# Performance work log

Measured on AMD Instinct MI355X. Metric: run time of the kernel, lower is better.

The kernel has to match this reference:

```python
import jax, jax.numpy as jnp
import numpy as np

H = 12          # num_heads
LENS_T = 64     # template tokens
LENS_S = 256    # search tokens
KEEP = int(0.7 * LENS_S)  # 179 kept search tokens


def _ln(x, s, b):
    mu = jnp.mean(x, axis=-1, keepdims=True)
    var = jnp.mean(jnp.square(x - mu), axis=-1, keepdims=True)
    return (x - mu) / jnp.sqrt(var + 1e-5) * s + b


def setup_inputs() -> dict:
    key = jax.random.key(0)
    ks = jax.random.split(key, 8)
    B, C, Hh = 32, 768, 3072
    N = LENS_T + LENS_S
    w = lambda k, shape: jax.random.normal(k, shape, jnp.float32) * 0.02
    return {
        "x": jax.random.normal(ks[0], (B, N, C), jnp.float32),
        "global_index_t": jnp.tile(jnp.arange(LENS_T, dtype=jnp.int32), (B, 1)),
        "global_index_s": jnp.tile(jnp.arange(LENS_S, dtype=jnp.int32), (B, 1)),
        "norm1_s": jnp.ones((C,), jnp.float32), "norm1_b": jnp.zeros((C,), jnp.float32),
        "qkv_w": w(ks[1], (C, 3 * C)), "qkv_b": jnp.zeros((3 * C,), jnp.float32),
        "proj_w": w(ks[2], (C, C)), "proj_b": jnp.zeros((C,), jnp.float32),
        "norm2_s": jnp.ones((C,), jnp.float32), "norm2_b": jnp.zeros((C,), jnp.float32),
        "fc1_w": w(ks[3], (C, Hh)), "fc1_b": jnp.zeros((Hh,), jnp.float32),
        "fc2_w": w(ks[4], (Hh, C)), "fc2_b": jnp.zeros((C,), jnp.float32),
        "gcn_w": w(ks[5], (C, C)), "gcn_b": jnp.zeros((C,), jnp.float32),
        "norm3_s": jnp.ones((C,), jnp.float32), "norm3_b": jnp.zeros((C,), jnp.float32),
    }


def reference(x, global_index_t, global_index_s,
              norm1_s, norm1_b, qkv_w, qkv_b, proj_w, proj_b,
              norm2_s, norm2_b, fc1_w, fc1_b, fc2_w, fc2_b,
              gcn_w, gcn_b, norm3_s, norm3_b):
    B, N, C = x.shape
    hd = C // H
    scale = hd ** -0.5

    # --- attention (attn weights explicitly materialized) ---
    h = _ln(x, norm1_s, norm1_b)
    qkv = (h @ qkv_w + qkv_b).reshape(B, N, 3, H, hd).transpose(2, 0, 3, 1, 4)
    q, k, v = qkv[0], qkv[1], qkv[2]                      # [B,H,N,hd]
    attn = jax.nn.softmax(jnp.einsum('bhqd,bhkd->bhqk', q, k) * scale, axis=-1)
    xa = jnp.einsum('bhqk,bhkd->bhqd', attn, v).transpose(0, 2, 1, 3).reshape(B, N, C)
    xa = xa @ proj_w + proj_b
    x = x + xa

    # --- MLP ---
    x_res = x
    h2 = _ln(x, norm2_s, norm2_b)
    h2 = jax.nn.gelu(h2 @ fc1_w + fc1_b, approximate=False) @ fc2_w + fc2_b
    x = x_res + h2

    # --- GCN using template<->search attention as adjacency ---
    # adjacency = [[0, w_ts], [w_ts^T, 0]]; exploit block sparsity instead of
    # materializing the dense [B,N,N] matrix.
    w_ts = jnp.sum(attn[:, :, :LENS_T, LENS_T:], axis=1) / H   # [B,T,S]
    w_ts = jax.nn.softmax(w_ts, axis=2)
    support = x @ gcn_w + gcn_b
    out_t = jnp.einsum('bts,bsd->btd', w_ts, support[:, LENS_T:])   # top block
    out_s = jnp.einsum('bts,btd->bsd', w_ts, support[:, :LENS_T])   # bottom block
    x = jnp.concatenate([out_t, out_s], axis=1)
    x = x + _ln(x, norm3_s, norm3_b)

    # --- top-k token pruning on search tokens ---
    score_s = jnp.mean(attn[:, :, :LENS_T, LENS_T:], axis=(1, 2))   # [B,S]
    order = jnp.argsort(-score_s, axis=1)
    keep_indices = order[:, :KEEP]
    removed_index_s = order[:, KEEP:]
    gs_new = jnp.take_along_axis(global_index_s, keep_indices, axis=1)
    idx = jnp.concatenate([global_index_t.astype(jnp.int32), keep_indices + LENS_T], axis=1)
    x = jnp.take_along_axis(x, jnp.broadcast_to(idx[..., None], (B, idx.shape[1], C)), axis=1)
    return (x, global_index_t, gs_new, removed_index_s, attn)
```

## Files before the change

kernel.cpp:

```cpp
#include <hip/hip_runtime.h>
#include <math.h>

#define NKEEP 179
#define NREM  77
#define NOUT_ROWS 243

typedef __bf16 bf16x8 __attribute__((ext_vector_type(8)));
typedef float f32x4 __attribute__((ext_vector_type(4)));

__device__ __forceinline__ unsigned short f2bf(float f) {
  unsigned u = __builtin_bit_cast(unsigned, f);
  u = (u + 0x7FFFu + ((u >> 16) & 1u)) >> 16;
  return (unsigned short)u;
}

__device__ __forceinline__ void gload_lds16(const void* g, void* l) {
  __builtin_amdgcn_global_load_lds((const __attribute__((address_space(1))) void*)g,
                                   (__attribute__((address_space(3))) void*)l,
                                   16, 0, 0);
}

template<int RESID, int OUTMODE>
__global__ __launch_bounds__(256)
void ln_kernel(const float* __restrict__ in, const float* __restrict__ gs,
               const float* __restrict__ gb, void* __restrict__ outp,
               void* __restrict__ outp2) {
  int row = blockIdx.x;
  const float* p = in + (size_t)row * 768;
  int tid = threadIdx.x;
  float v0 = p[tid], v1 = p[tid + 256], v2 = p[tid + 512];
  __shared__ double rs[256], rq[256];
  double d0 = v0, d1 = v1, d2 = v2;
  rs[tid] = d0 + d1 + d2;
  rq[tid] = d0 * d0 + d1 * d1 + d2 * d2;
  __syncthreads();
  for (int st = 128; st > 0; st >>= 1) {
    if (tid < st) { rs[tid] += rs[tid + st]; rq[tid] += rq[tid + st]; }
    __syncthreads();
  }
  double mu  = rs[0] * (1.0 / 768.0);
  double var = rq[0] * (1.0 / 768.0) - mu * mu;
  float rstd = (float)rsqrt(var + 1e-5);
  float muf = (float)mu;
  float y0 = (v0 - muf) * rstd * gs[tid]       + gb[tid];
  float y1 = (v1 - muf) * rstd * gs[tid + 256] + gb[tid + 256];
  float y2 = (v2 - muf) * rstd * gs[tid + 512] + gb[tid + 512];
  if (RESID) { y0 += v0; y1 += v1; y2 += v2; }
  if (OUTMODE == 0 || OUTMODE == 2) {
    float* o = (float*)outp + (size_t)row * 768;
    o[tid] = y0; o[tid + 256] = y1; o[tid + 512] = y2;
  }
  if (OUTMODE == 1) {
    unsigned short* o = (unsigned short*)outp + (size_t)row * 768;
    o[tid] = f2bf(y0); o[tid + 256] = f2bf(y1); o[tid + 512] = f2bf(y2);
  }
  if (OUTMODE == 2) {
    unsigned short* o = (unsigned short*)outp2 + (size_t)row * 768;
    o[tid] = f2bf(y0); o[tid + 256] = f2bf(y1); o[tid + 512] = f2bf(y2);
  }
}

__global__ __launch_bounds__(256)
void wtrans_kernel(const float* __restrict__ W, unsigned short* __restrict__ Wt,
                   int K, int N) {
  __shared__ float t[32][33];
  int n0 = blockIdx.x * 32, k0 = blockIdx.y * 32;
  int tid = threadIdx.x;
#pragma unroll
  for (int p = 0; p < 4; p++) {
    int idx = tid + p * 256;
    int r = idx >> 5, c = idx & 31;
    t[r][c] = W[(size_t)(k0 + r) * N + n0 + c];
  }
  __syncthreads();
#pragma unroll
  for (int p = 0; p < 4; p++) {
    int idx = tid + p * 256;
    int r = idx >> 5, c = idx & 31;
    Wt[(size_t)(n0 + r) * K + k0 + c] = f2bf(t[c][r]);
  }
}

template<int ACT, int RES, int OUTBF, int BN>
__global__ __launch_bounds__(256)
void gemm_bf16_kernel(const unsigned short* __restrict__ A,
                      const unsigned short* __restrict__ Bt,
                      const float* __restrict__ bias, const float* __restrict__ res,
                      void* __restrict__ outp, int M, int K, int N) {
  constexpr int NF = BN / 32;
  __shared__ unsigned short Al[128 * 64];
  __shared__ unsigned short Bl[BN * 64];
  int tid = threadIdx.x;
  int lane = tid & 63, wid = tid >> 6;
  int wr = wid >> 1, wc = wid & 1;
  int bm0 = blockIdx.x * 128, bn0 = blockIdx.y * BN;

  int r8 = lane >> 3;
  int csw = lane & 7;
  int csrc = csw ^ r8;

  const unsigned short* Abase = A + (size_t)bm0 * K + (size_t)csrc * 8;
  const unsigned short* Bbase = Bt + (size_t)bn0 * K + (size_t)csrc * 8;

  f32x4 acc[4][NF] = {};

  int mrow = lane & 15;
  int kch = lane >> 4;
  int key = mrow & 7;

  for (int k0 = 0; k0 < K; k0 += 64) {
#pragma unroll
    for (int i = 0; i < 4; i++) {
      int rr = wid * 32 + i * 8;
      gload_lds16(Abase + (size_t)(rr + r8) * K + k0, Al + rr * 64);
    }
#pragma unroll
    for (int i = 0; i < NF; i++) {
      int rr = wid * (BN / 4) + i * 8;
      gload_lds16(Bbase + (size_t)(rr + r8) * K + k0, Bl + rr * 64);
    }
    __syncthreads();
#pragma unroll
    for (int ks = 0; ks < 2; ks++) {
      bf16x8 af[4], bfr[NF];
#pragma unroll
      for (int f = 0; f < 4; f++) {
        int ra = wr * 64 + f * 16 + mrow;
        int ca = (ks * 4 + kch) ^ key;
        af[f] = *reinterpret_cast<const bf16x8*>(&Al[ra * 64 + ca * 8]);
      }
#pragma unroll
      for (int f = 0; f < NF; f++) {
        int ca = (ks * 4 + kch) ^ key;
        int rb = wc * (BN / 2) + f * 16 + mrow;
        bfr[f] = *reinterpret_cast<const bf16x8*>(&Bl[rb * 64 + ca * 8]);
      }
#pragma unroll
      for (int fm = 0; fm < 4; fm++)
#pragma unroll
        for (int fn = 0; fn < NF; fn++)
          acc[fm][fn] = __builtin_amdgcn_mfma_f32_16x16x32_bf16(
              af[fm], bfr[fn], acc[fm][fn], 0, 0, 0);
    }
    __syncthreads();
  }
#pragma unroll
  for (int fm = 0; fm < 4; fm++) {
#pragma unroll
    for (int j = 0; j < 4; j++) {
      int row = bm0 + wr * 64 + fm * 16 + (lane >> 4) * 4 + j;
#pragma unroll
      for (int fn = 0; fn < NF; fn++) {
        int col = bn0 + wc * (BN / 2) + fn * 16 + (lane & 15);
        float c = acc[fm][fn][j] + bias[col];
        if (ACT == 1) c = 0.5f * c * (1.0f + erff(c * 0.70710678118654752f));
        if (RES) c += res[(size_t)row * N + col];
        if (OUTBF) ((unsigned short*)outp)[(size_t)row * N + col] = f2bf(c);
        else       ((float*)outp)[(size_t)row * N + col] = c;
      }
    }
  }
}

__global__ __launch_bounds__(256)
void gemm_qkv_bf16_kernel(const unsigned short* __restrict__ A,
                          const unsigned short* __restrict__ Bt,
                          const float* __restrict__ bias,
                          float* __restrict__ Qb, float* __restrict__ Vb) {
  __shared__ unsigned short Al[128 * 64];
  __shared__ unsigned short Bl[128 * 64];
  const int K = 768;
  int tid = threadIdx.x;
  int lane = tid & 63, wid = tid >> 6;
  int wr = wid >> 1, wc = wid & 1;
  int by = blockIdx.y;
  int colbase = (by < 6) ? by * 128 : (by - 6) * 128 + 1536;
  int bm0 = blockIdx.x * 128;

  int r8 = lane >> 3;
  int csw = lane & 7;
  int csrc = csw ^ r8;

  const unsigned short* Abase = A + (size_t)bm0 * K + (size_t)csrc * 8;
  const unsigned short* Bbase = Bt + (size_t)colbase * K + (size_t)csrc * 8;

  f32x4 acc[4][4] = {};
  int mrow = lane & 15;
  int kch = lane >> 4;
  int key = mrow & 7;

  for (int k0 = 0; k0 < K; k0 += 64) {
#pragma unroll
    for (int i = 0; i < 4; i++) {
      int rr = wid * 32 + i * 8;
      gload_lds16(Abase + (size_t)(rr + r8) * K + k0, Al + rr * 64);
      gload_lds16(Bbase + (size_t)(rr + r8) * K + k0, Bl + rr * 64);
    }
    __syncthreads();
#pragma unroll
    for (int ks = 0; ks < 2; ks++) {
      bf16x8 af[4], bfr[4];
#pragma unroll
      for (int f = 0; f < 4; f++) {
        int ra = wr * 64 + f * 16 + mrow;
        int ca = (ks * 4 + kch) ^ key;
        af[f] = *reinterpret_cast<const bf16x8*>(&Al[ra * 64 + ca * 8]);
        int rb = wc * 64 + f * 16 + mrow;
        bfr[f] = *reinterpret_cast<const bf16x8*>(&Bl[rb * 64 + ca * 8]);
      }
#pragma unroll
      for (int fm = 0; fm < 4; fm++)
#pragma unroll
        for (int fn = 0; fn < 4; fn++)
          acc[fm][fn] = __builtin_amdgcn_mfma_f32_16x16x32_bf16(
              af[fm], bfr[fn], acc[fm][fn], 0, 0, 0);
    }
    __syncthreads();
  }
#pragma unroll
  for (int fm = 0; fm < 4; fm++) {
#pragma unroll
    for (int j = 0; j < 4; j++) {
      int row = bm0 + wr * 64 + fm * 16 + (lane >> 4) * 4 + j;
      int b = row / 320, nr = row - b * 320;
#pragma unroll
      for (int fn = 0; fn < 4; fn++) {
        int col = colbase + wc * 64 + fn * 16 + (lane & 15);
        int sel = col / 768;
        int rem = col - sel * 768;
        int h = rem >> 6, d = rem & 63;
        float* dstb = (sel == 0) ? Qb : Vb;
        dstb[(((size_t)(b * 12 + h) * 320 + nr) << 6) + d] = acc[fm][fn][j] + bias[col];
      }
    }
  }
}

template<int ROWMAP>
__global__ __launch_bounds__(256)
void gemm_prec_kernel(const float* __restrict__ A, const float* __restrict__ W,
                      const float* __restrict__ bias, int colOff,
                      float* __restrict__ Dst) {
  __shared__ float As[64 * 32];
  __shared__ float Bs[32 * 64];
  int tid = threadIdx.x;
  int lane = tid & 63, wid = tid >> 6;
  int tx = tid & 15, ty = tid >> 4;
  int bm0 = blockIdx.x * 64, bn0 = blockIdx.y * 64;

  int r8 = lane >> 3, csw = lane & 7, csrc = csw ^ r8;
  int aRowG[2];
#pragma unroll
  for (int i = 0; i < 2; i++) {
    int m = bm0 + wid * 16 + i * 8 + r8;
    aRowG[i] = ROWMAP ? ((m >> 6) * 320 + (m & 63)) : m;
  }
  int br8 = lane >> 4, cch = lane & 15;
  const float* WbaseL = W + colOff + bn0 + cch * 4;

  double master[4][4] = {};
  for (int k0 = 0; k0 < 768; k0 += 32) {
#pragma unroll
    for (int i = 0; i < 2; i++) {
      int rrA = wid * 16 + i * 8;
      gload_lds16(A + (size_t)aRowG[i] * 768 + k0 + csrc * 4, As + rrA * 32);
      int rrB = wid * 8 + i * 4;
      gload_lds16(WbaseL + (size_t)(k0 + rrB + br8) * 2304, Bs + rrB * 64);
    }
    __syncthreads();
#pragma unroll
    for (int half = 0; half < 2; half++) {
      float chunk[4][4] = {};
#pragma unroll
      for (int kg = 0; kg < 4; kg++) {
        int kc = half * 4 + kg;
        float4 a4[4];
#pragma unroll
        for (int i = 0; i < 4; i++) {
          int row = ty * 4 + i;
          a4[i] = *(const float4*)&As[row * 32 + ((kc ^ (row & 7)) << 2)];
        }
#pragma unroll
        for (int c = 0; c < 4; c++) {
          int kkk = kc * 4 + c;
          float4 bb = *(const float4*)&Bs[kkk * 64 + tx * 4];
          float aa[4];
#pragma unroll
          for (int i = 0; i < 4; i++)
            aa[i] = (c == 0) ? a4[i].x : (c == 1) ? a4[i].y
                  : (c == 2) ? a4[i].z : a4[i].w;
#pragma unroll
          for (int i = 0; i < 4; i++) {
            chunk[i][0] = fmaf(aa[i], bb.x, chunk[i][0]);
            chunk[i][1] = fmaf(aa[i], bb.y, chunk[i][1]);
            chunk[i][2] = fmaf(aa[i], bb.z, chunk[i][2]);
            chunk[i][3] = fmaf(aa[i], bb.w, chunk[i][3]);
          }
        }
      }
#pragma unroll
      for (int i = 0; i < 4; i++)
#pragma unroll
        for (int j = 0; j < 4; j++) master[i][j] += (double)chunk[i][j];
    }
    __syncthreads();
  }
  int n0 = bn0 + tx * 4;
  int h = n0 >> 6, d = n0 & 63;
#pragma unroll
  for (int i = 0; i < 4; i++) {
    int m = bm0 + ty * 4 + i;
    int b, nr;
    if (ROWMAP) { b = m >> 6; nr = m & 63; }
    else        { b = m / 320; nr = m - b * 320; }
    float* dst = Dst + (((size_t)(b * 12 + h) * 320 + nr) << 6) + d;
    float4 v;
    v.x = (float)master[i][0] + bias[colOff + n0];
    v.y = (float)master[i][1] + bias[colOff + n0 + 1];
    v.z = (float)master[i][2] + bias[colOff + n0 + 2];
    v.w = (float)master[i][3] + bias[colOff + n0 + 3];
    *(float4*)dst = v;
  }
}

__global__ __launch_bounds__(256)
void attn_fused_kernel(const float* __restrict__ Qb, const float* __restrict__ Kb,
                       const float* __restrict__ Vb, float* __restrict__ attn,
                       unsigned short* __restrict__ xa) {
  __shared__ float Qs[64][68];
  __shared__ float Ks[64][68];
  float (*Ps)[68] = Qs;
  int bid = blockIdx.x;
  int qt = bid / 384, bh = bid % 384;
  int h = bh % 12, b = bh / 12;
  int q0 = qt * 64;
  int t = threadIdx.x;
  int tx = t & 15, ty = t >> 4;
  const float* Qg = Qb + (((size_t)bh * 320 + q0) << 6);
  const float* Kg = Kb + (((size_t)bh * 320) << 6);
  const float* Vg = Vb + (((size_t)bh * 320) << 6);
  float* attn_bh = attn + ((size_t)bh * 320 + q0) * 320;

  {
    int r = t >> 2, c = (t & 3) * 16;
    const float* src = Qg + (r << 6) + c;
#pragma unroll
    for (int i = 0; i < 4; i++)
      *(float4*)&Qs[r][c + i * 4] = *(const float4*)(src + i * 4);
  }

  float s[4][20];
  float mrow[4] = {-1e30f, -1e30f, -1e30f, -1e30f};

#pragma unroll
  for (int kc = 0; kc < 5; ++kc) {
    __syncthreads();
    {
      int r = t >> 2, c = (t & 3) * 16;
      const float* src = Kg + ((size_t)(kc * 64 + r) << 6) + c;
#pragma unroll
      for (int i = 0; i < 4; i++)
        *(float4*)&Ks[r][c + i * 4] = *(const float4*)(src + i * 4);
    }
    __syncthreads();
    float acc[4][4] = {};
#pragma unroll 4
    for (int d0 = 0; d0 < 64; d0 += 4) {
      float4 qv[4], kv[4];
#pragma unroll
      for (int i = 0; i < 4; i++) qv[i] = *(const float4*)&Qs[ty * 4 + i][d0];
#pragma unroll
      for (int j = 0; j < 4; j++) kv[j] = *(const float4*)&Ks[tx * 4 + j][d0];
#pragma unroll
      for (int i = 0; i < 4; i++)
#pragma unroll
        for (int j = 0; j < 4; j++) {
          acc[i][j] = fmaf(qv[i].x, kv[j].x, acc[i][j]);
          acc[i][j] = fmaf(qv[i].y, kv[j].y, acc[i][j]);
          acc[i][j] = fmaf(qv[i].z, kv[j].z, acc[i][j]);
          acc[i][j] = fmaf(qv[i].w, kv[j].w, acc[i][j]);
        }
    }
#pragma unroll
    for (int i = 0; i < 4; i++) {
      float sx = acc[i][0] * 0.125f, sy = acc[i][1] * 0.125f;
      float sz = acc[i][2] * 0.125f, sw = acc[i][3] * 0.125f;
      mrow[i] = fmaxf(mrow[i], fmaxf(fmaxf(sx, sy), fmaxf(sz, sw)));
      s[i][kc * 4 + 0] = sx; s[i][kc * 4 + 1] = sy;
      s[i][kc * 4 + 2] = sz; s[i][kc * 4 + 3] = sw;
    }
  }
#pragma unroll
  for (int i = 0; i < 4; i++) {
    mrow[i] = fmaxf(mrow[i], __shfl_xor(mrow[i], 1, 16));
    mrow[i] = fmaxf(mrow[i], __shfl_xor(mrow[i], 2, 16));
    mrow[i] = fmaxf(mrow[i], __shfl_xor(mrow[i], 4, 16));
    mrow[i] = fmaxf(mrow[i], __shfl_xor(mrow[i], 8, 16));
  }

  double lsum[4] = {0.0, 0.0, 0.0, 0.0};
#pragma unroll
  for (int i = 0; i < 4; i++)
#pragma unroll
    for (int c = 0; c < 20; c++) {
      float e = expf(s[i][c] - mrow[i]);
      s[i][c] = e;
      lsum[i] += (double)e;
    }
#pragma unroll
  for (int i = 0; i < 4; i++) {
    lsum[i] += __shfl_xor(lsum[i], 1, 16);
    lsum[i] += __shfl_xor(lsum[i], 2, 16);
    lsum[i] += __shfl_xor(lsum[i], 4, 16);
    lsum[i] += __shfl_xor(lsum[i], 8, 16);
  }
  float inv[4];
#pragma unroll
  for (int i = 0; i < 4; i++) inv[i] = (float)(1.0 / lsum[i]);

#pragma unroll
  for (int i = 0; i < 4; i++)
#pragma unroll
    for (int kc = 0; kc < 5; kc++) {
      float4 sv;
      sv.x = s[i][kc * 4 + 0] * inv[i];
      sv.y = s[i][kc * 4 + 1] * inv[i];
      sv.z = s[i][kc * 4 + 2] * inv[i];
      sv.w = s[i][kc * 4 + 3] * inv[i];
      *(float4*)&attn_bh[(size_t)(ty * 4 + i) * 320 + kc * 64 + tx * 4] = sv;
    }

  float acc2[4][4] = {};
  for (int kc = 0; kc < 5; ++kc) {
    __syncthreads();
    {
      int r = t >> 2, c = (t & 3) * 16;
      const float* src = Vg + ((size_t)(kc * 64 + r) << 6) + c;
#pragma unroll
      for (int i = 0; i < 4; i++)
        *(float4*)&Ks[r][c + i * 4] = *(const float4*)(src + i * 4);
    }
#pragma unroll
    for (int i = 0; i < 4; i++) {
      float4 sv;
      sv.x = s[i][kc * 4 + 0] * inv[i];
      sv.y = s[i][kc * 4 + 1] * inv[i];
      sv.z = s[i][kc * 4 + 2] * inv[i];
      sv.w = s[i][kc * 4 + 3] * inv[i];
      *(float4*)&Ps[ty * 4 + i][tx * 4] = sv;
    }
    __syncthreads();
#pragma unroll 4
    for (int kk4 = 0; kk4 < 16; ++kk4) {
      float4 pv[4], vv[4];
#pragma unroll
      for (int i = 0; i < 4; i++)
        pv[i] = *(const float4*)&Ps[ty * 4 + i][kk4 * 4];
#pragma unroll
      for (int l = 0; l < 4; l++) vv[l] = *(const float4*)&Ks[kk4 * 4 + l][tx * 4];
#pragma unroll
      for (int i = 0; i < 4; i++) {
        acc2[i][0] = fmaf(pv[i].x, vv[0].x, acc2[i][0]);
        acc2[i][1] = fmaf(pv[i].x, vv[0].y, acc2[i][1]);
        acc2[i][2] = fmaf(pv[i].x, vv[0].z, acc2[i][2]);
        acc2[i][3] = fmaf(pv[i].x, vv[0].w, acc2[i][3]);
        acc2[i][0] = fmaf(pv[i].y, vv[1].x, acc2[i][0]);
        acc2[i][1] = fmaf(pv[i].y, vv[1].y, acc2[i][1]);
        acc2[i][2] = fmaf(pv[i].y, vv[1].z, acc2[i][2]);
        acc2[i][3] = fmaf(pv[i].y, vv[1].w, acc2[i][3]);
        acc2[i][0] = fmaf(pv[i].z, vv[2].x, acc2[i][0]);
        acc2[i][1] = fmaf(pv[i].z, vv[2].y, acc2[i][1]);
        acc2[i][2] = fmaf(pv[i].z, vv[2].z, acc2[i][2]);
        acc2[i][3] = fmaf(pv[i].z, vv[2].w, acc2[i][3]);
        acc2[i][0] = fmaf(pv[i].w, vv[3].x, acc2[i][0]);
        acc2[i][1] = fmaf(pv[i].w, vv[3].y, acc2[i][1]);
        acc2[i][2] = fmaf(pv[i].w, vv[3].z, acc2[i][2]);
        acc2[i][3] = fmaf(pv[i].w, vv[3].w, acc2[i][3]);
      }
    }
  }
#pragma unroll
  for (int i = 0; i < 4; i++) {
    unsigned short* dst = xa + (size_t)(b * 320 + q0 + ty * 4 + i) * 768 + h * 64 + tx * 4;
    uint2 pk;
    pk.x = (unsigned)f2bf(acc2[i][0]) | ((unsigned)f2bf(acc2[i][1]) << 16);
    pk.y = (unsigned)f2bf(acc2[i][2]) | ((unsigned)f2bf(acc2[i][3]) << 16);
    *(uint2*)dst = pk;
  }
}

__global__ __launch_bounds__(256)
void wts_kernel(const float* __restrict__ attn, float* __restrict__ wts) {
  int bid = blockIdx.x;
  int tt = bid & 63, b = bid >> 6;
  int s = threadIdx.x;
  float acc = 0.0f;
  const float* base = attn + (((size_t)(b * 12)) * 320 + tt) * 320 + 64 + s;
#pragma unroll
  for (int h = 0; h < 12; h++) acc += base[(size_t)h * 320 * 320];
  acc *= (1.0f / 12.0f);
  __shared__ float red[256];
  red[s] = acc; __syncthreads();
  for (int st = 128; st > 0; st >>= 1) {
    if (s < st) red[s] = fmaxf(red[s], red[s + st]);
    __syncthreads();
  }
  float m = red[0]; __syncthreads();
  float e = expf(acc - m);
  red[s] = e; __syncthreads();
  for (int st = 128; st > 0; st >>= 1) {
    if (s < st) red[s] += red[s + st];
    __syncthreads();
  }
  wts[(size_t)bid * 256 + s] = e / red[0];
}

__global__ __launch_bounds__(256)
void out_t_kernel(const float* __restrict__ wts, const float* __restrict__ sup,
                  float* __restrict__ x3) {
  int idx = blockIdx.x * 256 + threadIdx.x;
  int c = idx % 768;
  int tt = (idx / 768) % 64;
  int b = idx / (768 * 64);
  const float* wrow = wts + (size_t)(b * 64 + tt) * 256;
  const float* sp = sup + ((size_t)(b * 320 + 64)) * 768 + c;
  float acc = 0.0f;
  for (int s = 0; s < 256; s++) acc = fmaf(wrow[s], sp[(size_t)s * 768], acc);
  x3[((size_t)(b * 320 + tt)) * 768 + c] = acc;
}

__global__ __launch_bounds__(256)
void out_s_kernel(const float* __restrict__ wts, const float* __restrict__ sup,
                  float* __restrict__ x3) {
  int idx = blockIdx.x * 256 + threadIdx.x;
  int c = idx % 768;
  int s = (idx / 768) % 256;
  int b = idx / (768 * 256);
  const float* wp = wts + (size_t)(b * 64) * 256 + s;
  const float* sp = sup + ((size_t)(b * 320)) * 768 + c;
  float acc = 0.0f;
#pragma unroll 4
  for (int tt = 0; tt < 64; tt++) acc = fmaf(wp[(size_t)tt * 256], sp[(size_t)tt * 768], acc);
  x3[((size_t)(b * 320 + 64 + s)) * 768 + c] = acc;
}

__global__ __launch_bounds__(256)
void score_part_kernel(const float* __restrict__ attn, double* __restrict__ part) {
  int h = blockIdx.x, b = blockIdx.y;
  int s = threadIdx.x;
  const float* base = attn + (((size_t)(b * 12 + h)) * 320) * 320 + 64 + s;
  double acc = 0.0;
  for (int tt = 0; tt < 64; tt++) acc += (double)base[(size_t)tt * 320];
  part[((size_t)(b * 12 + h)) * 256 + s] = acc;
}

__global__ __launch_bounds__(256)
void score_final_kernel(const double* __restrict__ part, const int* __restrict__ git,
                        const int* __restrict__ gis, int* __restrict__ order_ws,
                        float* __restrict__ out_git, float* __restrict__ out_gs,
                        float* __restrict__ out_rm) {
  int b = blockIdx.x, s = threadIdx.x;
  double acc = 0.0;
#pragma unroll
  for (int h = 0; h < 12; h++) acc += part[((size_t)(b * 12 + h)) * 256 + s];
  __shared__ double sc[256];
  __shared__ int ord[256];
  sc[s] = acc;
  __syncthreads();
  double my = sc[s];
  int r = 0;
  for (int i = 0; i < 256; i++) {
    double si = sc[i];
    r += (si > my) || (si == my && i < s);
  }
  ord[r] = s;
  __syncthreads();
  int o = ord[s];
  order_ws[b * 256 + s] = o;
  if (s < NKEEP) out_gs[b * NKEEP + s] = (float)gis[b * 256 + o];
  else           out_rm[b * NREM + (s - NKEEP)] = (float)o;
  if (s < 64)    out_git[b * 64 + s] = (float)git[b * 64 + s];
}

__global__ __launch_bounds__(256)
void gather_kernel(const float* __restrict__ x3, const int* __restrict__ git,
                   const int* __restrict__ order_ws, float* __restrict__ out) {
  int bid = blockIdx.x;
  int j = bid % NOUT_ROWS, b = bid / NOUT_ROWS;
  int src = (j < 64) ? git[b * 64 + j] : (order_ws[b * 256 + (j - 64)] + 64);
  const float* p = x3 + ((size_t)(b * 320 + src)) * 768;
  float* o = out + ((size_t)(b * NOUT_ROWS + j)) * 768;
  int tid = threadIdx.x;
  o[tid] = p[tid]; o[tid + 256] = p[tid + 256]; o[tid + 512] = p[tid + 512];
}

extern "C" void kernel_launch(void* const* d_in, const int* in_sizes, int n_in,
                              void* d_out, int out_size, void* d_ws, size_t ws_size,
                              hipStream_t stream) {
  (void)in_sizes; (void)n_in; (void)out_size; (void)ws_size;
  const float* x      = (const float*)d_in[0];
  const int*   git    = (const int*)d_in[1];
  const int*   gis    = (const int*)d_in[2];
  const float* n1s    = (const float*)d_in[3];
  const float* n1b    = (const float*)d_in[4];
  const float* qkv_w  = (const float*)d_in[5];
  const float* qkv_b  = (const float*)d_in[6];
  const float* proj_w = (const float*)d_in[7];
  const float* proj_b = (const float*)d_in[8];
  const float* n2s    = (const float*)d_in[9];
  const float* n2b    = (const float*)d_in[10];
  const float* fc1_w  = (const float*)d_in[11];
  const float* fc1_b  = (const float*)d_in[12];
  const float* fc2_w  = (const float*)d_in[13];
  const float* fc2_b  = (const float*)d_in[14];
  const float* gcn_w  = (const float*)d_in[15];
  const float* gcn_b  = (const float*)d_in[16];
  const float* n3s    = (const float*)d_in[17];
  const float* n3b    = (const float*)d_in[18];

  float* out     = (float*)d_out;
  float* out_x   = out;
  float* out_git = out + 5971968;
  float* out_gs  = out + 5974016;
  float* out_rm  = out + 5979744;
  float* attn    = out + 5982208;

  float* w      = (float*)d_ws;
  float* bufA   = w;
  float* bufB   = w + 7864320;
  float* bufBIG = w + 15728640;
  float* Qbuf = bufBIG;
  float* Kbuf = bufBIG + 7864320;
  float* Vbuf = bufBIG + 15728640;
  unsigned short* ln1_bf = (unsigned short*)(bufBIG + 23592960);
  unsigned short* f1_bf = (unsigned short*)bufBIG;
  unsigned short* x2_bf = (unsigned short*)(bufBIG + 15728640);
  float* x3 = bufBIG + 19660800;
  unsigned short* wbf = (unsigned short*)(bufBIG + 27525120);
  unsigned short* proj_wt = wbf;
  unsigned short* fc1_wt  = wbf + 589824;
  unsigned short* fc2_wt  = fc1_wt + 2359296;
  unsigned short* gcn_wt  = fc2_wt + 2359296;
  unsigned short* qkv_wt  = gcn_wt + 589824;
  unsigned short* xa_bf = (unsigned short*)bufA;
  unsigned short* h2_bf = (unsigned short*)bufA;
  float* wts    = bufBIG + 31457280;
  int*   order_ws = (int*)(wts + 524288);
  double* partd  = (double*)(wts + 524288 + 8192);

  const int M = 10240;

  wtrans_kernel<<<dim3(24, 24), dim3(256), 0, stream>>>(proj_w, proj_wt, 768, 768);
  wtrans_kernel<<<dim3(96, 24), dim3(256), 0, stream>>>(fc1_w, fc1_wt, 768, 3072);
  wtrans_kernel<<<dim3(24, 96), dim3(256), 0, stream>>>(fc2_w, fc2_wt, 3072, 768);
  wtrans_kernel<<<dim3(24, 24), dim3(256), 0, stream>>>(gcn_w, gcn_wt, 768, 768);
  wtrans_kernel<<<dim3(72, 24), dim3(256), 0, stream>>>(qkv_w, qkv_wt, 768, 2304);

  ln_kernel<0, 2><<<dim3(M), dim3(256), 0, stream>>>(x, n1s, n1b, bufA, ln1_bf);
  gemm_qkv_bf16_kernel<<<dim3(80, 12), dim3(256), 0, stream>>>(
      ln1_bf, qkv_wt, qkv_b, Qbuf, Vbuf);
  gemm_prec_kernel<0><<<dim3(160, 12), dim3(256), 0, stream>>>(
      bufA, qkv_w, qkv_b, 768, Kbuf);
  gemm_prec_kernel<1><<<dim3(32, 12), dim3(256), 0, stream>>>(
      bufA, qkv_w, qkv_b, 0, Qbuf);
  attn_fused_kernel<<<dim3(1920), dim3(256), 0, stream>>>(
      Qbuf, Kbuf, Vbuf, attn, xa_bf);
  gemm_bf16_kernel<0, 1, 0, 64><<<dim3(M / 128, 768 / 64), dim3(256), 0, stream>>>(
      xa_bf, proj_wt, proj_b, x, bufB, M, 768, 768);
  ln_kernel<0, 1><<<dim3(M), dim3(256), 0, stream>>>(bufB, n2s, n2b, h2_bf, nullptr);
  gemm_bf16_kernel<1, 0, 1, 128><<<dim3(M / 128, 3072 / 128), dim3(256), 0, stream>>>(
      h2_bf, fc1_wt, fc1_b, nullptr, f1_bf, M, 768, 3072);
  gemm_bf16_kernel<0, 1, 1, 64><<<dim3(M / 128, 768 / 64), dim3(256), 0, stream>>>(
      f1_bf, fc2_wt, fc2_b, bufB, x2_bf, M, 3072, 768);
  wts_kernel<<<dim3(32 * 64), dim3(256), 0, stream>>>(attn, wts);
  gemm_bf16_kernel<0, 0, 0, 64><<<dim3(M / 128, 768 / 64), dim3(256), 0, stream>>>(
      x2_bf, gcn_wt, gcn_b, nullptr, bufA, M, 768, 768);
  out_t_kernel<<<dim3(32 * 64 * 768 / 256), dim3(256), 0, stream>>>(wts, bufA, x3);
  out_s_kernel<<<dim3(32 * 256 * 768 / 256), dim3(256), 0, stream>>>(wts, bufA, x3);
  ln_kernel<1, 0><<<dim3(M), dim3(256), 0, stream>>>(x3, n3s, n3b, x3, nullptr);
  score_part_kernel<<<dim3(12, 32), dim3(256), 0, stream>>>(attn, partd);
  score_final_kernel<<<dim3(32), dim3(256), 0, stream>>>(partd, git, gis, order_ws,
                                                         out_git, out_gs, out_rm);
  gather_kernel<<<dim3(32 * NOUT_ROWS), dim3(256), 0, stream>>>(x3, git,
                                                                order_ws, out_x);
}
```

Measured before the change: 969.4 us.

## Widen precise GEMM K-tile to 64 and interleave attention key columns

Result: no change. 969.3 us (-0.0%).

```diff
diff --git a/kernel.cpp b/kernel.cpp
--- a/kernel.cpp
+++ b/kernel.cpp
@@ -241,35 +241,37 @@
 void gemm_prec_kernel(const float* __restrict__ A, const float* __restrict__ W,
                       const float* __restrict__ bias, int colOff,
                       float* __restrict__ Dst) {
-  __shared__ float As[64 * 32];
-  __shared__ float Bs[32 * 64];
+  __shared__ float As[64 * 64];
+  __shared__ float Bs[64 * 64];
   int tid = threadIdx.x;
   int lane = tid & 63, wid = tid >> 6;
   int tx = tid & 15, ty = tid >> 4;
   int bm0 = blockIdx.x * 64, bn0 = blockIdx.y * 64;
 
-  int r8 = lane >> 3, csw = lane & 7, csrc = csw ^ r8;
-  int aRowG[2];
-#pragma unroll
-  for (int i = 0; i < 2; i++) {
-    int m = bm0 + wid * 16 + i * 8 + r8;
+  int r4 = lane >> 4, csw = lane & 15;
+  int aRowG[4];
+#pragma unroll
+  for (int i = 0; i < 4; i++) {
+    int m = bm0 + wid * 16 + i * 4 + r4;
     aRowG[i] = ROWMAP ? ((m >> 6) * 320 + (m & 63)) : m;
   }
-  int br8 = lane >> 4, cch = lane & 15;
-  const float* WbaseL = W + colOff + bn0 + cch * 4;
+  int aKey[4];
+#pragma unroll
+  for (int i = 0; i < 4; i++) aKey[i] = csw ^ ((wid * 16 + i * 4 + r4) & 7);
+  const float* WbaseL = W + colOff + bn0 + csw * 4;
 
   double master[4][4] = {};
-  for (int k0 = 0; k0 < 768; k0 += 32) {
-#pragma unroll
-    for (int i = 0; i < 2; i++) {
-      int rrA = wid * 16 + i * 8;
-      gload_lds16(A + (size_t)aRowG[i] * 768 + k0 + csrc * 4, As + rrA * 32);
-      int rrB = wid * 8 + i * 4;
-      gload_lds16(WbaseL + (size_t)(k0 + rrB + br8) * 2304, Bs + rrB * 64);
-    }
-    __syncthreads();
-#pragma unroll
-    for (int half = 0; half < 2; half++) {
+  for (int k0 = 0; k0 < 768; k0 += 64) {
+#pragma unroll
+    for (int i = 0; i < 4; i++) {
+      int rrA = wid * 16 + i * 4;
+      gload_lds16(A + (size_t)aRowG[i] * 768 + k0 + aKey[i] * 4, As + rrA * 64);
+      int rrB = wid * 16 + i * 4;
+      gload_lds16(WbaseL + (size_t)(k0 + rrB + r4) * 2304, Bs + rrB * 64);
+    }
+    __syncthreads();
+#pragma unroll
+    for (int half = 0; half < 4; half++) {
       float chunk[4][4] = {};
 #pragma unroll
       for (int kg = 0; kg < 4; kg++) {
@@ -278,7 +280,7 @@
 #pragma unroll
         for (int i = 0; i < 4; i++) {
           int row = ty * 4 + i;
-          a4[i] = *(const float4*)&As[row * 32 + ((kc ^ (row & 7)) << 2)];
+          a4[i] = *(const float4*)&As[row * 64 + ((kc ^ (row & 7)) << 2)];
         }
 #pragma unroll
         for (int c = 0; c < 4; c++) {
@@ -370,7 +372,7 @@
 #pragma unroll
       for (int i = 0; i < 4; i++) qv[i] = *(const float4*)&Qs[ty * 4 + i][d0];
 #pragma unroll
-      for (int j = 0; j < 4; j++) kv[j] = *(const float4*)&Ks[tx * 4 + j][d0];
+      for (int j = 0; j < 4; j++) kv[j] = *(const float4*)&Ks[j * 16 + tx][d0];
 #pragma unroll
       for (int i = 0; i < 4; i++)
 #pragma unroll
@@ -419,16 +421,14 @@
   for (int i = 0; i < 4; i++) inv[i] = (float)(1.0 / lsum[i]);
 
 #pragma unroll
-  for (int i = 0; i < 4; i++)
-#pragma unroll
-    for (int kc = 0; kc < 5; kc++) {
-      float4 sv;
-      sv.x = s[i][kc * 4 + 0] * inv[i];
-      sv.y = s[i][kc * 4 + 1] * inv[i];
-      sv.z = s[i][kc * 4 + 2] * inv[i];
-      sv.w = s[i][kc * 4 + 3] * inv[i];
-      *(float4*)&attn_bh[(size_t)(ty * 4 + i) * 320 + kc * 64 + tx * 4] = sv;
-    }
+  for (int i = 0; i < 4; i++) {
+    float* rp = attn_bh + (size_t)(ty * 4 + i) * 320;
+#pragma unroll
+    for (int kc = 0; kc < 5; kc++)
+#pragma unroll
+      for (int j = 0; j < 4; j++)
+        rp[kc * 64 + j * 16 + tx] = s[i][kc * 4 + j] * inv[i];
+  }
 
   float acc2[4][4] = {};
   for (int kc = 0; kc < 5; ++kc) {
@@ -441,14 +441,10 @@
         *(float4*)&Ks[r][c + i * 4] = *(const float4*)(src + i * 4);
     }
 #pragma unroll
-    for (int i = 0; i < 4; i++) {
-      float4 sv;
-      sv.x = s[i][kc * 4 + 0] * inv[i];
-      sv.y = s[i][kc * 4 + 1] * inv[i];
-      sv.z = s[i][kc * 4 + 2] * inv[i];
-      sv.w = s[i][kc * 4 + 3] * inv[i];
-      *(float4*)&Ps[ty * 4 + i][tx * 4] = sv;
-    }
+    for (int i = 0; i < 4; i++)
+#pragma unroll
+      for (int j = 0; j < 4; j++)
+        Ps[ty * 4 + i][j * 16 + tx] = s[i][kc * 4 + j] * inv[i];
     __syncthreads();
 #pragma unroll 4
     for (int kk4 = 0; kk4 < 16; ++kk4) {
```

## Split attention into fp32 template-query and bf16 MFMA search-query kernels

Applied to the files above, without the earlier changes.

Result: faster. 919.2 us (-5.2%).

```diff
diff --git a/kernel.cpp b/kernel.cpp
--- a/kernel.cpp
+++ b/kernel.cpp
@@ -103,7 +103,6 @@
   const unsigned short* Bbase = Bt + (size_t)bn0 * K + (size_t)csrc * 8;
 
   f32x4 acc[4][NF] = {};
-
   int mrow = lane & 15;
   int kch = lane >> 4;
   int key = mrow & 7;
@@ -166,15 +165,17 @@
 void gemm_qkv_bf16_kernel(const unsigned short* __restrict__ A,
                           const unsigned short* __restrict__ Bt,
                           const float* __restrict__ bias,
-                          float* __restrict__ Qb, float* __restrict__ Vb) {
+                          unsigned short* __restrict__ Qbf,
+                          unsigned short* __restrict__ Kbf,
+                          float* __restrict__ Vb,
+                          unsigned short* __restrict__ Vtbf) {
   __shared__ unsigned short Al[128 * 64];
   __shared__ unsigned short Bl[128 * 64];
   const int K = 768;
   int tid = threadIdx.x;
   int lane = tid & 63, wid = tid >> 6;
   int wr = wid >> 1, wc = wid & 1;
-  int by = blockIdx.y;
-  int colbase = (by < 6) ? by * 128 : (by - 6) * 128 + 1536;
+  int colbase = blockIdx.y * 128;
   int bm0 = blockIdx.x * 128;
 
   int r8 = lane >> 3;
@@ -220,17 +221,37 @@
 #pragma unroll
   for (int fm = 0; fm < 4; fm++) {
 #pragma unroll
-    for (int j = 0; j < 4; j++) {
-      int row = bm0 + wr * 64 + fm * 16 + (lane >> 4) * 4 + j;
-      int b = row / 320, nr = row - b * 320;
-#pragma unroll
-      for (int fn = 0; fn < 4; fn++) {
-        int col = colbase + wc * 64 + fn * 16 + (lane & 15);
-        int sel = col / 768;
-        int rem = col - sel * 768;
-        int h = rem >> 6, d = rem & 63;
-        float* dstb = (sel == 0) ? Qb : Vb;
-        dstb[(((size_t)(b * 12 + h) * 320 + nr) << 6) + d] = acc[fm][fn][j] + bias[col];
+    for (int fn = 0; fn < 4; fn++) {
+      int col = colbase + wc * 64 + fn * 16 + (lane & 15);
+      int sel = col / 768;
+      int rem = col - sel * 768;
+      int h = rem >> 6, d = rem & 63;
+      int row0 = bm0 + wr * 64 + fm * 16 + (lane >> 4) * 4;
+      int b = row0 / 320, nr0 = row0 - b * 320;
+      size_t bh = (size_t)(b * 12 + h);
+      float v0 = acc[fm][fn][0] + bias[col];
+      float v1 = acc[fm][fn][1] + bias[col];
+      float v2 = acc[fm][fn][2] + bias[col];
+      float v3 = acc[fm][fn][3] + bias[col];
+      if (sel == 0) {
+        Qbf[(bh * 320 + nr0 + 0) * 64 + d] = f2bf(v0);
+        Qbf[(bh * 320 + nr0 + 1) * 64 + d] = f2bf(v1);
+        Qbf[(bh * 320 + nr0 + 2) * 64 + d] = f2bf(v2);
+        Qbf[(bh * 320 + nr0 + 3) * 64 + d] = f2bf(v3);
+      } else if (sel == 1) {
+        Kbf[(bh * 320 + nr0 + 0) * 64 + d] = f2bf(v0);
+        Kbf[(bh * 320 + nr0 + 1) * 64 + d] = f2bf(v1);
+        Kbf[(bh * 320 + nr0 + 2) * 64 + d] = f2bf(v2);
+        Kbf[(bh * 320 + nr0 + 3) * 64 + d] = f2bf(v3);
+      } else {
+        Vb[(bh * 320 + nr0 + 0) * 64 + d] = v0;
+        Vb[(bh * 320 + nr0 + 1) * 64 + d] = v1;
+        Vb[(bh * 320 + nr0 + 2) * 64 + d] = v2;
+        Vb[(bh * 320 + nr0 + 3) * 64 + d] = v3;
+        uint2 pk;
+        pk.x = (unsigned)f2bf(v0) | ((unsigned)f2bf(v1) << 16);
+        pk.y = (unsigned)f2bf(v2) | ((unsigned)f2bf(v3) << 16);
+        *(uint2*)&Vtbf[(bh * 64 + d) * 320 + nr0] = pk;
       }
     }
   }
@@ -310,36 +331,36 @@
 #pragma unroll
   for (int i = 0; i < 4; i++) {
     int m = bm0 + ty * 4 + i;
-    int b, nr;
-    if (ROWMAP) { b = m >> 6; nr = m & 63; }
-    else        { b = m / 320; nr = m - b * 320; }
-    float* dst = Dst + (((size_t)(b * 12 + h) * 320 + nr) << 6) + d;
     float4 v;
     v.x = (float)master[i][0] + bias[colOff + n0];
     v.y = (float)master[i][1] + bias[colOff + n0 + 1];
     v.z = (float)master[i][2] + bias[colOff + n0 + 2];
     v.w = (float)master[i][3] + bias[colOff + n0 + 3];
-    *(float4*)dst = v;
-  }
-}
-
-__global__ __launch_bounds__(256)
-void attn_fused_kernel(const float* __restrict__ Qb, const float* __restrict__ Kb,
-                       const float* __restrict__ Vb, float* __restrict__ attn,
-                       unsigned short* __restrict__ xa) {
+    if (ROWMAP) {
+      int b = m >> 6, nr = m & 63;
+      *(float4*)(Dst + (((size_t)(b * 12 + h) * 64 + nr) << 6) + d) = v;
+    } else {
+      int b = m / 320, nr = m - b * 320;
+      *(float4*)(Dst + (((size_t)(b * 12 + h) * 320 + nr) << 6) + d) = v;
+    }
+  }
+}
+
+__global__ __launch_bounds__(256)
+void attn_t_kernel(const float* __restrict__ Qt, const float* __restrict__ Kb,
+                   const float* __restrict__ Vb, float* __restrict__ attn,
+                   unsigned short* __restrict__ xa) {
   __shared__ float Qs[64][68];
   __shared__ float Ks[64][68];
   float (*Ps)[68] = Qs;
-  int bid = blockIdx.x;
-  int qt = bid / 384, bh = bid % 384;
+  int bh = blockIdx.x;
   int h = bh % 12, b = bh / 12;
-  int q0 = qt * 64;
   int t = threadIdx.x;
   int tx = t & 15, ty = t >> 4;
-  const float* Qg = Qb + (((size_t)bh * 320 + q0) << 6);
+  const float* Qg = Qt + (size_t)bh * 4096;
   const float* Kg = Kb + (((size_t)bh * 320) << 6);
   const float* Vg = Vb + (((size_t)bh * 320) << 6);
-  float* attn_bh = attn + ((size_t)bh * 320 + q0) * 320;
+  float* attn_bh = attn + ((size_t)bh * 320) * 320;
 
   {
     int r = t >> 2, c = (t & 3) * 16;
@@ -370,7 +391,7 @@
 #pragma unroll
       for (int i = 0; i < 4; i++) qv[i] = *(const float4*)&Qs[ty * 4 + i][d0];
 #pragma unroll
-      for (int j = 0; j < 4; j++) kv[j] = *(const float4*)&Ks[tx * 4 + j][d0];
+      for (int j = 0; j < 4; j++) kv[j] = *(const float4*)&Ks[j * 16 + tx][d0];
 #pragma unroll
       for (int i = 0; i < 4; i++)
 #pragma unroll
@@ -419,16 +440,14 @@
   for (int i = 0; i < 4; i++) inv[i] = (float)(1.0 / lsum[i]);
 
 #pragma unroll
-  for (int i = 0; i < 4; i++)
-#pragma unroll
-    for (int kc = 0; kc < 5; kc++) {
-      float4 sv;
-      sv.x = s[i][kc * 4 + 0] * inv[i];
-      sv.y = s[i][kc * 4 + 1] * inv[i];
-      sv.z = s[i][kc * 4 + 2] * inv[i];
-      sv.w = s[i][kc * 4 + 3] * inv[i];
-      *(float4*)&attn_bh[(size_t)(ty * 4 + i) * 320 + kc * 64 + tx * 4] = sv;
-    }
+  for (int i = 0; i < 4; i++) {
+    float* rp = attn_bh + (size_t)(ty * 4 + i) * 320;
+#pragma unroll
+    for (int kc = 0; kc < 5; kc++)
+#pragma unroll
+      for (int j = 0; j < 4; j++)
+        rp[kc * 64 + j * 16 + tx] = s[i][kc * 4 + j] * inv[i];
+  }
 
   float acc2[4][4] = {};
   for (int kc = 0; kc < 5; ++kc) {
@@ -441,14 +460,10 @@
         *(float4*)&Ks[r][c + i * 4] = *(const float4*)(src + i * 4);
     }
 #pragma unroll
-    for (int i = 0; i < 4; i++) {
-      float4 sv;
-      sv.x = s[i][kc * 4 + 0] * inv[i];
-      sv.y = s[i][kc * 4 + 1] * inv[i];
-      sv.z = s[i][kc * 4 + 2] * inv[i];
-      sv.w = s[i][kc * 4 + 3] * inv[i];
-      *(float4*)&Ps[ty * 4 + i][tx * 4] = sv;
-    }
+    for (int i = 0; i < 4; i++)
+#pragma unroll
+      for (int j = 0; j < 4; j++)
+        Ps[ty * 4 + i][j * 16 + tx] = s[i][kc * 4 + j] * inv[i];
     __syncthreads();
 #pragma unroll 4
     for (int kk4 = 0; kk4 < 16; ++kk4) {
@@ -481,12 +496,149 @@
   }
 #pragma unroll
   for (int i = 0; i < 4; i++) {
-    unsigned short* dst = xa + (size_t)(b * 320 + q0 + ty * 4 + i) * 768 + h * 64 + tx * 4;
+    unsigned short* dst = xa + (size_t)(b * 320 + ty * 4 + i) * 768 + h * 64 + tx * 4;
     uint2 pk;
     pk.x = (unsigned)f2bf(acc2[i][0]) | ((unsigned)f2bf(acc2[i][1]) << 16);
     pk.y = (unsigned)f2bf(acc2[i][2]) | ((unsigned)f2bf(acc2[i][3]) << 16);
     *(uint2*)dst = pk;
   }
+}
+
+__global__ __launch_bounds__(256)
+void attn_s_kernel(const unsigned short* __restrict__ Qbf,
+                   const unsigned short* __restrict__ Kbf,
+                   const unsigned short* __restrict__ Vtbf,
+                   float* __restrict__ attn, unsigned short* __restrict__ xa) {
+  __shared__ unsigned short lds_[24576];
+  unsigned short* Ql  = lds_;
+  unsigned short* Kl  = lds_ + 4096;
+  unsigned short* Pl  = lds_;
+  unsigned short* Vtl = lds_ + 20480;
+
+  int bid = blockIdx.x;
+  int sqt = bid / 384, bh = bid % 384;
+  int h = bh % 12, b = bh / 12;
+  int q0 = 64 + sqt * 64;
+  int tid = threadIdx.x;
+  int lane = tid & 63, wid = tid >> 6;
+  int r8 = lane >> 3, csw = lane & 7, csrc = csw ^ r8;
+  int mrow = lane & 15, kch = lane >> 4, key = mrow & 7;
+
+  const unsigned short* Qg = Qbf + ((size_t)bh * 320 + q0) * 64 + csrc * 8;
+  const unsigned short* Kg = Kbf + (size_t)bh * 320 * 64 + csrc * 8;
+#pragma unroll
+  for (int i = 0; i < 2; i++) {
+    int rr = wid * 16 + i * 8;
+    gload_lds16(Qg + (size_t)(rr + r8) * 64, Ql + rr * 64);
+  }
+#pragma unroll
+  for (int i = 0; i < 10; i++) {
+    int rr = wid * 80 + i * 8;
+    gload_lds16(Kg + (size_t)(rr + r8) * 64, Kl + rr * 64);
+  }
+  __syncthreads();
+
+  bf16x8 af[2];
+#pragma unroll
+  for (int ks = 0; ks < 2; ks++)
+    af[ks] = *reinterpret_cast<const bf16x8*>(
+        &Ql[(wid * 16 + mrow) * 64 + (((ks * 4 + kch) ^ key) << 3)]);
+  f32x4 acc[20] = {};
+#pragma unroll
+  for (int nt = 0; nt < 20; nt++) {
+#pragma unroll
+    for (int ks = 0; ks < 2; ks++) {
+      bf16x8 bk = *reinterpret_cast<const bf16x8*>(
+          &Kl[(nt * 16 + mrow) * 64 + (((ks * 4 + kch) ^ key) << 3)]);
+      acc[nt] = __builtin_amdgcn_mfma_f32_16x16x32_bf16(af[ks], bk, acc[nt], 0, 0, 0);
+    }
+  }
+
+  float m4[4] = {-1e30f, -1e30f, -1e30f, -1e30f};
+#pragma unroll
+  for (int nt = 0; nt < 20; nt++)
+#pragma unroll
+    for (int j = 0; j < 4; j++) {
+      acc[nt][j] *= 0.125f;
+      m4[j] = fmaxf(m4[j], acc[nt][j]);
+    }
+#pragma unroll
+  for (int j = 0; j < 4; j++) {
+    m4[j] = fmaxf(m4[j], __shfl_xor(m4[j], 1, 16));
+    m4[j] = fmaxf(m4[j], __shfl_xor(m4[j], 2, 16));
+    m4[j] = fmaxf(m4[j], __shfl_xor(m4[j], 4, 16));
+    m4[j] = fmaxf(m4[j], __shfl_xor(m4[j], 8, 16));
+  }
+  float s4[4] = {0.0f, 0.0f, 0.0f, 0.0f};
+#pragma unroll
+  for (int nt = 0; nt < 20; nt++)
+#pragma unroll
+    for (int j = 0; j < 4; j++) {
+      float e = expf(acc[nt][j] - m4[j]);
+      acc[nt][j] = e;
+      s4[j] += e;
+    }
+#pragma unroll
+  for (int j = 0; j < 4; j++) {
+    s4[j] += __shfl_xor(s4[j], 1, 16);
+    s4[j] += __shfl_xor(s4[j], 2, 16);
+    s4[j] += __shfl_xor(s4[j], 4, 16);
+    s4[j] += __shfl_xor(s4[j], 8, 16);
+  }
+  float inv4[4];
+#pragma unroll
+  for (int j = 0; j < 4; j++) inv4[j] = 1.0f / s4[j];
+
+  __syncthreads();
+
+  float* attn_q = attn + ((size_t)bh * 320 + q0) * 320;
+#pragma unroll
+  for (int j = 0; j < 4; j++) {
+    int r = wid * 16 + (lane >> 4) * 4 + j;
+    float* rp = attn_q + (size_t)r * 320;
+    int rkey = r & 7;
+#pragma unroll
+    for (int nt = 0; nt < 20; nt++) {
+      float p = acc[nt][j] * inv4[j];
+      int k = nt * 16 + mrow;
+      rp[k] = p;
+      int c = k >> 3;
+      int cs = (c & 0x38) | ((c ^ rkey) & 7);
+      Pl[r * 320 + cs * 8 + (k & 7)] = f2bf(p);
+    }
+  }
+
+  f32x4 acc2[4] = {};
+  const unsigned short* Vg = Vtbf + (size_t)bh * 64 * 320 + csrc * 8;
+  for (int kc = 0; kc < 5; kc++) {
+    __syncthreads();
+#pragma unroll
+    for (int i = 0; i < 2; i++) {
+      int rr = wid * 16 + i * 8;
+      gload_lds16(Vg + (size_t)(rr + r8) * 320 + kc * 64, Vtl + rr * 64);
+    }
+    __syncthreads();
+#pragma unroll
+    for (int ks = 0; ks < 2; ks++) {
+      int cc = (ks * 4 + kch) ^ key;
+      bf16x8 ap = *reinterpret_cast<const bf16x8*>(
+          &Pl[(wid * 16 + mrow) * 320 + ((kc * 8 + cc) << 3)]);
+#pragma unroll
+      for (int nd = 0; nd < 4; nd++) {
+        bf16x8 bv = *reinterpret_cast<const bf16x8*>(
+            &Vtl[(nd * 16 + mrow) * 64 + (cc << 3)]);
+        acc2[nd] = __builtin_amdgcn_mfma_f32_16x16x32_bf16(ap, bv, acc2[nd], 0, 0, 0);
+      }
+    }
+  }
+#pragma unroll
+  for (int nd = 0; nd < 4; nd++)
+#pragma unroll
+    for (int j = 0; j < 4; j++) {
+      int r = wid * 16 + (lane >> 4) * 4 + j;
+      int d = nd * 16 + mrow;
+      xa[((size_t)(b * 320) + q0 + r) * 768 + h * 64 + d] = f2bf(acc2[nd][j]);
+    }
 }
 
 __global__ __launch_bounds__(256)
@@ -629,10 +781,13 @@
   float* bufA   = w;
   float* bufB   = w + 7864320;
   float* bufBIG = w + 15728640;
-  float* Qbuf = bufBIG;
+  float* Qt   = bufBIG;
+  unsigned short* Vtbf = (unsigned short*)(bufBIG + 1572864);
   float* Kbuf = bufBIG + 7864320;
   float* Vbuf = bufBIG + 15728640;
   unsigned short* ln1_bf = (unsigned short*)(bufBIG + 23592960);
+  unsigned short* Qbf = (unsigned short*)bufB;
+  unsigned short* Kbf = (unsigned short*)(bufB + 3932160);
   unsigned short* f1_bf = (unsigned short*)bufBIG;
   unsigned short* x2_bf = (unsigned short*)(bufBIG + 15728640);
   float* x3 = bufBIG + 19660800;
@@ -657,14 +812,16 @@
   wtrans_kernel<<<dim3(72, 24), dim3(256), 0, stream>>>(qkv_w, qkv_wt, 768, 2304);
 
   ln_kernel<0, 2><<<dim3(M), dim3(256), 0, stream>>>(x, n1s, n1b, bufA, ln1_bf);
-  gemm_qkv_bf16_kernel<<<dim3(80, 12), dim3(256), 0, stream>>>(
-      ln1_bf, qkv_wt, qkv_b, Qbuf, Vbuf);
+  gemm_qkv_bf16_kernel<<<dim3(80, 18), dim3(256), 0, stream>>>(
+      ln1_bf, qkv_wt, qkv_b, Qbf, Kbf, Vbuf, Vtbf);
   gemm_prec_kernel<0><<<dim3(160, 12), dim3(256), 0, stream>>>(
       bufA, qkv_w, qkv_b, 768, Kbuf);
   gemm_prec_kernel<1><<<dim3(32, 12), dim3(256), 0, stream>>>(
-      bufA, qkv_w, qkv_b, 0, Qbuf);
-  attn_fused_kernel<<<dim3(1920), dim3(256), 0, stream>>>(
-      Qbuf, Kbuf, Vbuf, attn, xa_bf);
+      bufA, qkv_w, qkv_b, 0, Qt);
+  attn_t_kernel<<<dim3(384), dim3(256), 0, stream>>>(
+      Qt, Kbuf, Vbuf, attn, xa_bf);
+  attn_s_kernel<<<dim3(1536), dim3(256), 0, stream>>>(
+      Qbf, Kbf, Vtbf, attn, xa_bf);
   gemm_bf16_kernel<0, 1, 0, 64><<<dim3(M / 128, 768 / 64), dim3(256), 0, stream>>>(
       xa_bf, proj_wt, proj_b, x, bufB, M, 768, 768);
   ln_kernel<0, 1><<<dim3(M), dim3(256), 0, stream>>>(bufB, n2s, n2b, h2_bf, nullptr);
```
